# Kernel tuning notes

Measured on AMD Instinct MI355X. Metric: run time of the kernel, lower is better.

Reference implementation:

```python
import jax, jax.numpy as jnp
import numpy as np

N, CIN, T, V = 16, 16, 512, 200
K, COUT, H = 3, 64, 64


def setup_inputs() -> dict:
    key = jax.random.key(0)
    ks = jax.random.split(key, 9)
    s = 0.05
    return {
        "x": jax.random.normal(ks[0], (N, CIN, T, V), jnp.float32),
        "A": jax.random.uniform(ks[1], (K, V, V), jnp.float32) / V,
        "W_gcn": jax.random.normal(ks[2], (K * COUT, CIN), jnp.float32) * s,
        "b_gcn": jnp.zeros((K * COUT,), jnp.float32),
        "W_ih": jax.random.normal(ks[3], (4 * H, COUT), jnp.float32) * s,
        "W_hh": jax.random.normal(ks[4], (4 * H, H), jnp.float32) * s,
        "b_ih": jnp.zeros((4 * H,), jnp.float32),
        "b_hh": jnp.zeros((4 * H,), jnp.float32),
        "W_fc": jax.random.normal(ks[5], (1, H), jnp.float32) * s,
        "b_fc": jnp.zeros((1,), jnp.float32),
    }


def reference(x, A, W_gcn, b_gcn, W_ih, W_hh, b_ih, b_hh, W_fc, b_fc):
    n, c, t, v = x.shape
    k = A.shape[0]
    cout = W_gcn.shape[0] // k
    # ConvTemporalGraphical: 1x1 conv -> (n, k*cout, t, v), reshape, adjacency einsum
    y = jnp.einsum('nctv,oc->notv', x, W_gcn) + b_gcn[None, :, None, None]
    y = y.reshape(n, k, cout, t, v)
    y = jnp.einsum('nkctv,kvw->nctw', y, A)  # (n, cout, t, v)
    # mean over node dim, residual=False -> res=0
    y = jnp.mean(y, axis=3)  # (n, cout, t)
    seq = jnp.transpose(y, (2, 0, 1))  # (t, n, cout) time-major for scan

    def step(carry, xt):
        h, ccell = carry
        gates = xt @ W_ih.T + b_ih + h @ W_hh.T + b_hh  # (n, 4H)
        i, f, g, o = jnp.split(gates, 4, axis=-1)  # torch LSTM gate order
        i = jax.nn.sigmoid(i)
        f = jax.nn.sigmoid(f)
        g = jnp.tanh(g)
        o = jax.nn.sigmoid(o)
        ccell = f * ccell + i * g
        h = o * jnp.tanh(ccell)
        return (h, ccell), None

    h0 = jnp.zeros((n, W_hh.shape[1]), x.dtype)
    (h_last, _), _ = jax.lax.scan(step, (h0, h0), seq)
    out = h_last @ W_fc.T + b_fc  # (n, 1)
    return (out, A)
```

## Files before the change

kernel.cpp:

```cpp
#include <hip/hip_runtime.h>
#include <math.h>

#define N_    16
#define CIN_  16
#define T_    512
#define V_    200
#define K_    3
#define COUT_ 64
#define H_    64
#define G_    256

#define WS_A  0
#define WS_SA 640
#define WS_XA 1024
#define WS_XW (WS_XA + N_ * T_ * K_ * CIN_)

__device__ __forceinline__ float fast_sig(float x) {
    return __builtin_amdgcn_rcpf(1.f + __expf(-x));
}
__device__ __forceinline__ float fast_tanh(float x) {
    return fmaf(-2.f, __builtin_amdgcn_rcpf(1.f + __expf(2.f * x)), 1.f);
}

__global__ __launch_bounds__(256) void prep_kernel(const float* __restrict__ A,
                                                   float* __restrict__ out,
                                                   float* __restrict__ ws) {
    int tid = blockIdx.x * blockDim.x + threadIdx.x;
    if (tid < K_ * V_ * V_) out[16 + tid] = A[tid];
    if (tid < K_ * V_) {
        const float* row = A + (long)tid * V_;
        float s = 0.f;
        for (int w = 0; w < V_; ++w) s += row[w];
        ws[WS_A + tid] = s * (1.0f / V_);
    }
}

__global__ void sa_kernel(float* __restrict__ ws) {
    int k = threadIdx.x;
    if (k < K_) {
        float s = 0.f;
        for (int v = 0; v < V_; ++v) s += ws[WS_A + k * V_ + v];
        ws[WS_SA + k] = s;
    }
}

__global__ __launch_bounds__(256) void xa_kernel(const float* __restrict__ x,
                                                 float* __restrict__ ws) {
    __shared__ float aS[K_ * V_];
    int tid = threadIdx.x;
    for (int i = tid; i < K_ * V_; i += 256) aS[i] = ws[WS_A + i];
    __syncthreads();

    int wave = tid >> 6, lane = tid & 63;
    int row = blockIdx.x * 4 + wave;
    const float* xr = x + (long)row * V_;

    float s0 = 0.f, s1 = 0.f, s2 = 0.f;
    for (int v = lane; v < V_; v += 64) {
        float xv = xr[v];
        s0 = fmaf(xv, aS[v], s0);
        s1 = fmaf(xv, aS[V_ + v], s1);
        s2 = fmaf(xv, aS[2 * V_ + v], s2);
    }
    #pragma unroll
    for (int m = 1; m < 64; m <<= 1) {
        s0 += __shfl_xor(s0, m);
        s1 += __shfl_xor(s1, m);
        s2 += __shfl_xor(s2, m);
    }
    if (lane == 0) {
        int t  = row % T_;
        int nc = row / T_;
        int ci = nc % CIN_;
        int n  = nc / CIN_;
        long base = (long)(n * T_ + t) * (K_ * CIN_);
        ws[WS_XA + base + 0 * CIN_ + ci] = s0;
        ws[WS_XA + base + 1 * CIN_ + ci] = s1;
        ws[WS_XA + base + 2 * CIN_ + ci] = s2;
    }
}

__global__ __launch_bounds__(256) void gates_pre_kernel(
    const float* __restrict__ W_gcn, const float* __restrict__ b_gcn,
    const float* __restrict__ W_ih, const float* __restrict__ b_ih,
    const float* __restrict__ b_hh, float* __restrict__ ws) {
    int nt = blockIdx.x;
    int t = nt % T_, n = nt / T_;
    __shared__ float xaS[K_ * CIN_];
    __shared__ float seqS[COUT_];
    int tid = threadIdx.x;
    if (tid < K_ * CIN_)
        xaS[tid] = ws[WS_XA + (long)(n * T_ + t) * (K_ * CIN_) + tid];
    __syncthreads();
    if (tid < COUT_) {
        float s = 0.f;
        #pragma unroll
        for (int k = 0; k < K_; ++k) {
            s = fmaf(b_gcn[k * COUT_ + tid], ws[WS_SA + k], s);
            const float* wrow = W_gcn + (long)(k * COUT_ + tid) * CIN_;
            #pragma unroll
            for (int ci = 0; ci < CIN_; ++ci)
                s = fmaf(wrow[ci], xaS[k * CIN_ + ci], s);
        }
        seqS[tid] = s;
    }
    __syncthreads();
    float g = b_ih[tid] + b_hh[tid];
    const float* wrow = W_ih + (long)tid * H_;
    #pragma unroll 8
    for (int c = 0; c < H_; ++c) g = fmaf(wrow[c], seqS[c], g);
    ws[WS_XW + (long)(t * N_ + n) * G_ + tid] = g;
}

__global__ __launch_bounds__(256, 1) void lstm_kernel(
    const float* __restrict__ W_hh, const float* __restrict__ W_fc,
    const float* __restrict__ b_fc, const float* __restrict__ ws,
    float* __restrict__ out) {
    int n = blockIdx.x;
    int w = threadIdx.x >> 6;
    int lane = threadIdx.x & 63;

    const float4* wr = (const float4*)(W_hh + (long)(w * H_ + lane) * H_);
    float4 w0  = wr[0],  w1  = wr[1],  w2  = wr[2],  w3  = wr[3];
    float4 w4  = wr[4],  w5  = wr[5],  w6  = wr[6],  w7  = wr[7];
    float4 w8  = wr[8],  w9  = wr[9],  w10 = wr[10], w11 = wr[11];
    float4 w12 = wr[12], w13 = wr[13], w14 = wr[14], w15 = wr[15];

    __shared__ __align__(16) float hS[H_];
    __shared__ float gbuf[4][H_];

    if (threadIdx.x < H_) hS[threadIdx.x] = 0.f;
    float ccell = 0.f, hlast = 0.f;
    __syncthreads();

    const float* xw = ws + WS_XW + (long)n * G_ + (w * H_ + lane);
    float x0 = xw[0];
    float x1 = xw[(long)N_ * G_];

    for (int t = 0; t < T_; ++t) {
        float gate = x0;
        x0 = x1;
        if (t + 2 < T_) x1 = xw[(long)(t + 2) * N_ * G_];

        float a0 = 0.f, a1 = 0.f, a2 = 0.f, a3 = 0.f;
        const float4* h4 = (const float4*)hS;
        #define DOT4(i)                          \
            {                                    \
                float4 hv = h4[i];               \
                a0 = fmaf(w##i.x, hv.x, a0);     \
                a1 = fmaf(w##i.y, hv.y, a1);     \
                a2 = fmaf(w##i.z, hv.z, a2);     \
                a3 = fmaf(w##i.w, hv.w, a3);     \
            }
        DOT4(0)  DOT4(1)  DOT4(2)  DOT4(3)
        DOT4(4)  DOT4(5)  DOT4(6)  DOT4(7)
        DOT4(8)  DOT4(9)  DOT4(10) DOT4(11)
        DOT4(12) DOT4(13) DOT4(14) DOT4(15)
        #undef DOT4
        gate += (a0 + a1) + (a2 + a3);

        gbuf[w][lane] = gate;
        __syncthreads();
        if (w == 0) {
            float iv = fast_sig(gate);
            float fv = fast_sig(gbuf[1][lane]);
            float gv = fast_tanh(gbuf[2][lane]);
            float ov = fast_sig(gbuf[3][lane]);
            ccell = fmaf(fv, ccell, iv * gv);
            hlast = ov * fast_tanh(ccell);
            hS[lane] = hlast;
        }
        __syncthreads();
    }

    if (w == 0) {
        float p = hlast * W_fc[lane];
        #pragma unroll
        for (int m = 1; m < 64; m <<= 1) p += __shfl_xor(p, m);
        if (lane == 0) out[n] = p + b_fc[0];
    }
}

extern "C" void kernel_launch(void* const* d_in, const int* in_sizes, int n_in,
                              void* d_out, int out_size, void* d_ws, size_t ws_size,
                              hipStream_t stream) {
    const float* x     = (const float*)d_in[0];
    const float* A     = (const float*)d_in[1];
    const float* W_gcn = (const float*)d_in[2];
    const float* b_gcn = (const float*)d_in[3];
    const float* W_ih  = (const float*)d_in[4];
    const float* W_hh  = (const float*)d_in[5];
    const float* b_ih  = (const float*)d_in[6];
    const float* b_hh  = (const float*)d_in[7];
    const float* W_fc  = (const float*)d_in[8];
    const float* b_fc  = (const float*)d_in[9];
    float* out = (float*)d_out;
    float* ws  = (float*)d_ws;

    int copy_elems = K_ * V_ * V_;
    prep_kernel<<<(copy_elems + 255) / 256, 256, 0, stream>>>(A, out, ws);
    sa_kernel<<<1, 64, 0, stream>>>(ws);
    int rows = N_ * CIN_ * T_;
    xa_kernel<<<rows / 4, 256, 0, stream>>>(x, ws);
    gates_pre_kernel<<<N_ * T_, 256, 0, stream>>>(W_gcn, b_gcn, W_ih, b_ih, b_hh, ws);
    lstm_kernel<<<N_, 256, 0, stream>>>(W_hh, W_fc, b_fc, ws, out);
}
```

Measured before the change: 402.2 us.

## Batch gate precompute across samples per timestep and fold sa into prep

```diff
diff --git a/kernel.cpp b/kernel.cpp
--- a/kernel.cpp
+++ b/kernel.cpp
@@ -22,25 +22,32 @@
     return fmaf(-2.f, __builtin_amdgcn_rcpf(1.f + __expf(2.f * x)), 1.f);
 }
 
+#define NCOPY ((K_ * V_ * V_ + 255) / 256)
 __global__ __launch_bounds__(256) void prep_kernel(const float* __restrict__ A,
                                                    float* __restrict__ out,
                                                    float* __restrict__ ws) {
-    int tid = blockIdx.x * blockDim.x + threadIdx.x;
-    if (tid < K_ * V_ * V_) out[16 + tid] = A[tid];
-    if (tid < K_ * V_) {
-        const float* row = A + (long)tid * V_;
+    int b = blockIdx.x;
+    if (b < NCOPY) {
+        int tid = b * 256 + threadIdx.x;
+        if (tid < K_ * V_ * V_) out[16 + tid] = A[tid];
+        if (tid < K_ * V_) {
+            const float* row = A + (long)tid * V_;
+            float s = 0.f;
+            for (int w = 0; w < V_; ++w) s += row[w];
+            ws[WS_A + tid] = s * (1.0f / V_);
+        }
+    } else {
+        int k = b - NCOPY;
+        const float* Ak = A + (long)k * V_ * V_;
         float s = 0.f;
-        for (int w = 0; w < V_; ++w) s += row[w];
-        ws[WS_A + tid] = s * (1.0f / V_);
-    }
-}
-
-__global__ void sa_kernel(float* __restrict__ ws) {
-    int k = threadIdx.x;
-    if (k < K_) {
-        float s = 0.f;
-        for (int v = 0; v < V_; ++v) s += ws[WS_A + k * V_ + v];
-        ws[WS_SA + k] = s;
+        for (int i = threadIdx.x; i < V_ * V_; i += 256) s += Ak[i];
+        #pragma unroll
+        for (int m = 1; m < 64; m <<= 1) s += __shfl_xor(s, m);
+        __shared__ float red[4];
+        if ((threadIdx.x & 63) == 0) red[threadIdx.x >> 6] = s;
+        __syncthreads();
+        if (threadIdx.x == 0)
+            ws[WS_SA + k] = (red[0] + red[1] + red[2] + red[3]) * (1.0f / V_);
     }
 }
 
@@ -80,36 +87,69 @@
     }
 }
 
-__global__ __launch_bounds__(256) void gates_pre_kernel(
+__global__ __launch_bounds__(256) void seqgates_kernel(
     const float* __restrict__ W_gcn, const float* __restrict__ b_gcn,
     const float* __restrict__ W_ih, const float* __restrict__ b_ih,
     const float* __restrict__ b_hh, float* __restrict__ ws) {
-    int nt = blockIdx.x;
-    int t = nt % T_, n = nt / T_;
-    __shared__ float xaS[K_ * CIN_];
-    __shared__ float seqS[COUT_];
+    int t = blockIdx.x;
     int tid = threadIdx.x;
-    if (tid < K_ * CIN_)
-        xaS[tid] = ws[WS_XA + (long)(n * T_ + t) * (K_ * CIN_) + tid];
-    __syncthreads();
-    if (tid < COUT_) {
-        float s = 0.f;
-        #pragma unroll
-        for (int k = 0; k < K_; ++k) {
-            s = fmaf(b_gcn[k * COUT_ + tid], ws[WS_SA + k], s);
-            const float* wrow = W_gcn + (long)(k * COUT_ + tid) * CIN_;
+    __shared__ float xaS[N_][K_ * CIN_];
+    __shared__ __align__(16) float seqS[N_][COUT_];
+    __shared__ float saS[K_];
+
+    if (tid < K_) saS[tid] = ws[WS_SA + tid];
+    #pragma unroll
+    for (int r = 0; r < 3; ++r) {
+        int i = tid + r * 256;
+        if (i < N_ * K_ * CIN_) {
+            int n = i / (K_ * CIN_), kc = i % (K_ * CIN_);
+            xaS[n][kc] = ws[WS_XA + (long)(n * T_ + t) * (K_ * CIN_) + kc];
+        }
+    }
+    __syncthreads();
+
+    {
+        int n = tid >> 4, c0 = (tid & 15) * 4;
+        #pragma unroll
+        for (int cc = 0; cc < 4; ++cc) {
+            int c = c0 + cc;
+            float s = 0.f;
             #pragma unroll
-            for (int ci = 0; ci < CIN_; ++ci)
-                s = fmaf(wrow[ci], xaS[k * CIN_ + ci], s);
-        }
-        seqS[tid] = s;
-    }
-    __syncthreads();
-    float g = b_ih[tid] + b_hh[tid];
-    const float* wrow = W_ih + (long)tid * H_;
-    #pragma unroll 8
-    for (int c = 0; c < H_; ++c) g = fmaf(wrow[c], seqS[c], g);
-    ws[WS_XW + (long)(t * N_ + n) * G_ + tid] = g;
+            for (int k = 0; k < K_; ++k) {
+                s = fmaf(b_gcn[k * COUT_ + c], saS[k], s);
+                const float* wrow = W_gcn + (long)(k * COUT_ + c) * CIN_;
+                #pragma unroll
+                for (int ci = 0; ci < CIN_; ++ci)
+                    s = fmaf(wrow[ci], xaS[n][k * CIN_ + ci], s);
+            }
+            seqS[n][c] = s;
+        }
+    }
+    __syncthreads();
+
+    {
+        int g = tid;
+        float acc[N_];
+        #pragma unroll
+        for (int n = 0; n < N_; ++n) acc[n] = 0.f;
+        const float4* wrow4 = (const float4*)(W_ih + (long)g * H_);
+        #pragma unroll
+        for (int c4 = 0; c4 < H_ / 4; ++c4) {
+            float4 w4 = wrow4[c4];
+            #pragma unroll
+            for (int n = 0; n < N_; ++n) {
+                float4 s4 = ((const float4*)seqS[n])[c4];
+                acc[n] = fmaf(w4.x, s4.x, acc[n]);
+                acc[n] = fmaf(w4.y, s4.y, acc[n]);
+                acc[n] = fmaf(w4.z, s4.z, acc[n]);
+                acc[n] = fmaf(w4.w, s4.w, acc[n]);
+            }
+        }
+        float bias = b_ih[g] + b_hh[g];
+        #pragma unroll
+        for (int n = 0; n < N_; ++n)
+            ws[WS_XW + (long)(t * N_ + n) * G_ + g] = acc[n] + bias;
+    }
 }
 
 __global__ __launch_bounds__(256, 1) void lstm_kernel(
@@ -197,11 +237,9 @@
     float* out = (float*)d_out;
     float* ws  = (float*)d_ws;
 
-    int copy_elems = K_ * V_ * V_;
-    prep_kernel<<<(copy_elems + 255) / 256, 256, 0, stream>>>(A, out, ws);
-    sa_kernel<<<1, 64, 0, stream>>>(ws);
+    prep_kernel<<<NCOPY + K_, 256, 0, stream>>>(A, out, ws);
     int rows = N_ * CIN_ * T_;
     xa_kernel<<<rows / 4, 256, 0, stream>>>(x, ws);
-    gates_pre_kernel<<<N_ * T_, 256, 0, stream>>>(W_gcn, b_gcn, W_ih, b_ih, b_hh, ws);
+    seqgates_kernel<<<T_, 256, 0, stream>>>(W_gcn, b_gcn, W_ih, b_ih, b_hh, ws);
     lstm_kernel<<<N_, 256, 0, stream>>>(W_hh, W_fc, b_fc, ws, out);
 }
```

After: 385.9 us. 1.04x faster.
